# Performance work log

Measured on AMD Instinct MI355X. Metric: run time of the kernel, lower is better.

The kernel has to match this reference:

```python
import jax, jax.numpy as jnp
import numpy as np

B, T, K = 2048, 120, 128


def setup_inputs() -> dict:
    key = jax.random.key(0)
    k1, k2, k3 = jax.random.split(key, 3)
    emissions = jax.random.normal(k1, (B, T, K), dtype=jnp.float32)
    tag_ids = jax.random.randint(k2, (B, T), 0, K, dtype=jnp.int64)
    mask = jnp.ones((B, T), dtype=jnp.int32)  # full-length sequences
    # learned CRF transition weight (orthogonal-init stand-in: scaled normal)
    transitions = jax.random.normal(k3, (K, K), dtype=jnp.float32) * 0.1
    return {"emissions": emissions, "tag_ids": tag_ids, "mask": mask,
            "transitions": transitions}


def _crf_neg_log_likelihood(emissions, tag_ids, mask, transitions):
    maskf = mask.astype(emissions.dtype)  # [B,T]
    # ---- gold path score ----
    # unary: emission score of the gold tag at each valid position
    unary = jnp.take_along_axis(emissions, tag_ids[..., None], axis=2)[..., 0]  # [B,T]
    unary_score = jnp.sum(unary * maskf, axis=1)  # [B]
    # binary: transition score between consecutive gold tags (both positions valid)
    trans = transitions[tag_ids[:, :-1], tag_ids[:, 1:]]  # [B,T-1]
    pair_mask = maskf[:, :-1] * maskf[:, 1:]
    binary_score = jnp.sum(trans * pair_mask, axis=1)  # [B]
    score = unary_score + binary_score  # [B]

    # ---- log partition via forward algorithm (sequential scan over time) ----
    alpha0 = emissions[:, 0, :]  # [B,K]

    def step(alpha, xs):
        emis_t, mask_t = xs  # [B,K], [B]
        # alpha[b,i] + transitions[i,j] -> logsumexp over i, add emission at t
        new_alpha = jax.nn.logsumexp(alpha[:, :, None] + transitions[None, :, :],
                                     axis=1) + emis_t  # [B,K]
        alpha = jnp.where(mask_t[:, None] > 0, new_alpha, alpha)
        return alpha, None

    xs = (jnp.swapaxes(emissions[:, 1:, :], 0, 1),  # [T-1,B,K]
          jnp.swapaxes(mask[:, 1:], 0, 1))          # [T-1,B]
    alpha, _ = jax.lax.scan(step, alpha0, xs)
    log_norm = jax.nn.logsumexp(alpha, axis=1)  # [B]

    log_likelihood = score - log_norm  # [B]
    return -jnp.mean(log_likelihood)


def reference(emissions, tag_ids, mask, transitions):
    # CrfLossLayer.call computes the CRF NLL loss (added via add_loss);
    # the padded emissions/mask outputs are trivial zero-pads of the inputs.
    return _crf_neg_log_likelihood(emissions, tag_ids, mask, transitions)
```

## Files before the change

kernel.cpp:

```cpp
#include <hip/hip_runtime.h>
#include <cstddef>
#include <cstdint>

typedef __attribute__((ext_vector_type(8))) _Float16 half8;
typedef __attribute__((ext_vector_type(4))) float f32x4;

constexpr int Bsz = 2048, Tsz = 120, Ksz = 128;
constexpr float L2E = 1.44269504088896340736f;
constexpr float LN2 = 0.69314718055994530942f;

__device__ __forceinline__ int expbits(float x) {
  return (int)(__float_as_uint(x) >> 23) - 127;
}

#define BAR() do {                                        \
    asm volatile("s_waitcnt lgkmcnt(0)" ::: "memory");    \
    __builtin_amdgcn_s_barrier();                         \
    __builtin_amdgcn_sched_barrier(0);                    \
  } while (0)

__global__ __launch_bounds__(256) void crf_fwd(
    const float* __restrict__ emis,
    const int* __restrict__ tag,
    const int* __restrict__ maskg,
    const float* __restrict__ Tg,
    float* __restrict__ nll)
{
  __shared__ float Tst[Ksz * Ksz];
  __shared__ __align__(16) uint2 Pb[2][16 * 32];
  __shared__ __align__(16) float lamp[2][16][20];
  __shared__ int maskLds[Tsz * 16];

  const int tid = threadIdx.x;
  const int w = tid >> 6, lane = tid & 63;
  const int c = lane & 15, hi = lane >> 4;
  const int b0 = blockIdx.x * 16;
  const int sw2 = (c & 7) << 1;
  const int slot = 4 * w + hi;

  const int soff = 32 * w + 4 * hi;
  const float* ep = emis + (size_t)(b0 + c) * Tsz * Ksz + soff;

  f32x4 a0[2], emA[2], emB[2];
  a0[0] = *(const f32x4*)(ep);
  a0[1] = *(const f32x4*)(ep + 16);
  emA[0] = *(const f32x4*)(ep + Ksz);
  emA[1] = *(const f32x4*)(ep + Ksz + 16);
  emB[0] = *(const f32x4*)(ep + 2 * Ksz);
  emB[1] = *(const f32x4*)(ep + 2 * Ksz + 16);

  {
    const f32x4* src = (const f32x4*)Tg;
    f32x4* dst = (f32x4*)Tst;
    #pragma unroll
    for (int k = 0; k < (Ksz * Ksz / 4) / 256; ++k)
      dst[tid + k * 256] = src[tid + k * 256];
  }
  for (int i = tid; i < Tsz * 16; i += 256) {
    int cc = i & 15, tt = i >> 4;
    maskLds[i] = maskg[(size_t)(b0 + cc) * Tsz + tt];
  }
  __syncthreads();

  half8 Ef[2][4];
  #pragma unroll
  for (int rti = 0; rti < 2; ++rti)
    #pragma unroll
    for (int m = 0; m < 4; ++m) {
      half8 v;
      #pragma unroll
      for (int j = 0; j < 8; ++j)
        v[j] = (_Float16)__expf(Tst[(32 * m + 8 * hi + j) * Ksz + (32 * w + 16 * rti + c)]);
      Ef[rti][m] = v;
    }

  {
    float pm = fmaxf(fmaxf(fmaxf(a0[0][0], a0[0][1]), fmaxf(a0[0][2], a0[0][3])),
                     fmaxf(fmaxf(a0[1][0], a0[1][1]), fmaxf(a0[1][2], a0[1][3])));
    lamp[1][c][slot] = pm;
  }
  BAR();
  float nReg;
  f32x4 Pv[2];
  {
    const float* lr = &lamp[1][c][0];
    f32x4 l0 = *(const f32x4*)(lr), l1 = *(const f32x4*)(lr + 4);
    f32x4 l2 = *(const f32x4*)(lr + 8), l3 = *(const f32x4*)(lr + 12);
    f32x4 mm;
    #pragma unroll
    for (int r = 0; r < 4; ++r) mm[r] = fmaxf(fmaxf(l0[r], l1[r]), fmaxf(l2[r], l3[r]));
    float mx = fmaxf(fmaxf(mm[0], mm[1]), fmaxf(mm[2], mm[3]));
    nReg = mx * L2E;
    #pragma unroll
    for (int rti = 0; rti < 2; ++rti)
      #pragma unroll
      for (int r = 0; r < 4; ++r) Pv[rti][r] = __expf(a0[rti][r] - mx);
  }

  auto publish = [&](int wr) {
    float pl = 0.f;
    #pragma unroll
    for (int rti = 0; rti < 2; ++rti) {
      union { _Float16 h[4]; uint2 u; } pk;
      #pragma unroll
      for (int r = 0; r < 4; ++r) {
        pk.h[r] = (_Float16)Pv[rti][r];
        pl = fmaxf(pl, Pv[rti][r]);
      }
      Pb[wr][c * 32 + ((8 * w + 4 * rti + hi) ^ sw2)] = pk.u;
    }
    lamp[wr][c][slot] = pl;
  };

  publish(0);
  BAR();

  const f32x4 z = {0.f, 0.f, 0.f, 0.f};

  auto STEP = [&](int t, f32x4 (&em)[2]) {
    const int rd = (t - 1) & 1, wr = t & 1;
    const uint2* prowR = &Pb[rd][c * 32];
    half8 bf[4];
    #pragma unroll
    for (int m = 0; m < 4; ++m) {
      union { uint4 u4; half8 h; } rb;
      const int idx = (8 * m + 2 * hi) ^ sw2;
      rb.u4 = *(const uint4*)(&prowR[idx]);
      bf[m] = rb.h;
    }
    const float* lr = &lamp[rd][c][0];
    f32x4 l0 = *(const f32x4*)(lr), l1 = *(const f32x4*)(lr + 4);
    f32x4 l2 = *(const f32x4*)(lr + 8), l3 = *(const f32x4*)(lr + 12);
    f32x4 mm;
    #pragma unroll
    for (int r = 0; r < 4; ++r) mm[r] = fmaxf(fmaxf(l0[r], l1[r]), fmaxf(l2[r], l3[r]));
    const float lam = fmaxf(fmaxf(mm[0], mm[1]), fmaxf(mm[2], mm[3]));
    const int Dfi = expbits(lam) + 8;
    const float s2 = __uint_as_float((uint32_t)(127 - Dfi) << 23);
    const int mt = maskLds[t * 16 + c];

    f32x4 eem[2];
    #pragma unroll
    for (int rti = 0; rti < 2; ++rti)
      #pragma unroll
      for (int r = 0; r < 4; ++r) eem[rti][r] = __expf(em[rti][r]);

    f32x4 acc[2];
    #pragma unroll
    for (int rti = 0; rti < 2; ++rti) {
      f32x4 aA = __builtin_amdgcn_mfma_f32_16x16x32_f16(
          Ef[rti][1], bf[1],
          __builtin_amdgcn_mfma_f32_16x16x32_f16(Ef[rti][0], bf[0], z, 0, 0, 0),
          0, 0, 0);
      f32x4 aB = __builtin_amdgcn_mfma_f32_16x16x32_f16(
          Ef[rti][3], bf[3],
          __builtin_amdgcn_mfma_f32_16x16x32_f16(Ef[rti][2], bf[2], z, 0, 0, 0),
          0, 0, 0);
      #pragma unroll
      for (int r = 0; r < 4; ++r) acc[rti][r] = aA[r] + aB[r];
    }

    if (t + 2 < Tsz) {
      em[0] = *(const f32x4*)(ep + (size_t)(t + 2) * Ksz);
      em[1] = *(const f32x4*)(ep + (size_t)(t + 2) * Ksz + 16);
    }

    f32x4 c2[2];
    #pragma unroll
    for (int rti = 0; rti < 2; ++rti)
      #pragma unroll
      for (int r = 0; r < 4; ++r) c2[rti][r] = eem[rti][r] * s2;

    unsigned long long bal = __ballot(mt > 0);
    if (bal == ~0ull) {
      #pragma unroll
      for (int rti = 0; rti < 2; ++rti)
        #pragma unroll
        for (int r = 0; r < 4; ++r) Pv[rti][r] = acc[rti][r] * c2[rti][r];
    } else {
      #pragma unroll
      for (int rti = 0; rti < 2; ++rti)
        #pragma unroll
        for (int r = 0; r < 4; ++r) {
          float pn = acc[rti][r] * c2[rti][r];
          float po = Pv[rti][r] * s2;
          Pv[rti][r] = (mt > 0) ? pn : po;
        }
    }
    nReg += (float)Dfi;

    publish(wr);
    BAR();
  };

  #pragma unroll 1
  for (int t = 1; t <= Tsz - 3; t += 2) {
    STEP(t, emA);
    STEP(t + 1, emB);
  }
  STEP(Tsz - 1, emA);

  {
    float ss = ((Pv[0][0] + Pv[0][1]) + (Pv[0][2] + Pv[0][3]))
             + ((Pv[1][0] + Pv[1][1]) + (Pv[1][2] + Pv[1][3]));
    lamp[1][c][slot] = ss;
  }
  BAR();
  float lognorm;
  {
    const float* lr = &lamp[1][c][0];
    f32x4 l0 = *(const f32x4*)(lr), l1 = *(const f32x4*)(lr + 4);
    f32x4 l2 = *(const f32x4*)(lr + 8), l3 = *(const f32x4*)(lr + 12);
    float tot = (((l0[0] + l0[1]) + (l0[2] + l0[3]))
              + ((l1[0] + l1[1]) + (l1[2] + l1[3])))
              + (((l2[0] + l2[1]) + (l2[2] + l2[3]))
              + ((l3[0] + l3[1]) + (l3[2] + l3[3])));
    lognorm = nReg * LN2 + __logf(tot);
  }

  {
    const int* tb = tag + (size_t)(b0 + c) * Tsz;
    const float* eb2 = emis + (size_t)(b0 + c) * Tsz * Ksz;
    float sc = 0.f;
    const int t0 = 8 * slot;
    const int t1 = (t0 + 8 < Tsz) ? t0 + 8 : Tsz;
    #pragma unroll 1
    for (int t = t0; t < t1; ++t) {
      int tg0 = tb[t];
      float m0 = (float)maskLds[t * 16 + c];
      sc += eb2[(size_t)t * Ksz + tg0] * m0;
      if (t + 1 < Tsz) {
        int tg1 = tb[t + 1];
        sc += Tst[tg0 * Ksz + tg1] * m0 * (float)maskLds[(t + 1) * 16 + c];
      }
    }
    float* scb = (float*)&Pb[0][0];
    scb[c * 16 + slot] = sc;
    BAR();
    if (tid < 16) {
      const float* sr = &scb[c * 16];
      float s2r = 0.f;
      #pragma unroll
      for (int s = 0; s < 16; ++s) s2r += sr[s];
      nll[b0 + c] = lognorm - s2r;
    }
  }
}

__global__ __launch_bounds__(256) void crf_reduce(
    const float* __restrict__ nll, float* __restrict__ out) {
  __shared__ float buf[256];
  float s = 0.f;
  for (int i = threadIdx.x; i < Bsz; i += 256) s += nll[i];
  buf[threadIdx.x] = s;
  __syncthreads();
  #pragma unroll
  for (int off = 128; off > 0; off >>= 1) {
    if (threadIdx.x < off) buf[threadIdx.x] += buf[threadIdx.x + off];
    __syncthreads();
  }
  if (threadIdx.x == 0) out[0] = buf[0] / (float)Bsz;
}

extern "C" void kernel_launch(void* const* d_in, const int* in_sizes, int n_in,
                              void* d_out, int out_size, void* d_ws, size_t ws_size,
                              hipStream_t stream) {
  const float* emissions   = (const float*)d_in[0];
  const int*   tag_ids     = (const int*)d_in[1];
  const int*   mask        = (const int*)d_in[2];
  const float* transitions = (const float*)d_in[3];

  float* nll = (float*)d_ws;

  crf_fwd<<<Bsz / 16, 256, 0, stream>>>(emissions, tag_ids, mask, transitions, nll);
  crf_reduce<<<1, 256, 0, stream>>>(nll, (float*)d_out);
}
```

Before: 78.27 us.

## Halve block to two waves, each computing 64 tags per step

Each block now uses 128 threads (2 waves), and each wave covers 64 output tags with 4 MFMA column tiles instead of 2. This cuts the per-step barrier and LDS max-reduction cost, since 8 slots are reduced instead of 16. The transition matrix is no longer staged in LDS; the exp table and gold-path transition lookups read global memory directly. Emission loads are prefetched three steps ahead and their exp is computed before each step, which raises register pressure and halves the number of waves available per block.

```diff
diff --git a/kernel.cpp b/kernel.cpp
--- a/kernel.cpp
+++ b/kernel.cpp
@@ -16,19 +16,18 @@
 #define BAR() do {                                        \
     asm volatile("s_waitcnt lgkmcnt(0)" ::: "memory");    \
     __builtin_amdgcn_s_barrier();                         \
-    __builtin_amdgcn_sched_barrier(0);                    \
+    asm volatile("" ::: "memory");                        \
   } while (0)
 
-__global__ __launch_bounds__(256) void crf_fwd(
+__global__ __launch_bounds__(128, 1) void crf_fwd(
     const float* __restrict__ emis,
     const int* __restrict__ tag,
     const int* __restrict__ maskg,
     const float* __restrict__ Tg,
     float* __restrict__ nll)
 {
-  __shared__ float Tst[Ksz * Ksz];
   __shared__ __align__(16) uint2 Pb[2][16 * 32];
-  __shared__ __align__(16) float lamp[2][16][20];
+  __shared__ __align__(16) float lamp[2][16][10];
   __shared__ int maskLds[Tsz * 16];
 
   const int tid = threadIdx.x;
@@ -38,76 +37,76 @@
   const int sw2 = (c & 7) << 1;
   const int slot = 4 * w + hi;
 
-  const int soff = 32 * w + 4 * hi;
+  const int soff = 64 * w + 4 * hi;
   const float* ep = emis + (size_t)(b0 + c) * Tsz * Ksz + soff;
 
-  f32x4 a0[2], emA[2], emB[2];
-  a0[0] = *(const f32x4*)(ep);
-  a0[1] = *(const f32x4*)(ep + 16);
-  emA[0] = *(const f32x4*)(ep + Ksz);
-  emA[1] = *(const f32x4*)(ep + Ksz + 16);
-  emB[0] = *(const f32x4*)(ep + 2 * Ksz);
-  emB[1] = *(const f32x4*)(ep + 2 * Ksz + 16);
-
-  {
-    const f32x4* src = (const f32x4*)Tg;
-    f32x4* dst = (f32x4*)Tst;
-    #pragma unroll
-    for (int k = 0; k < (Ksz * Ksz / 4) / 256; ++k)
-      dst[tid + k * 256] = src[tid + k * 256];
-  }
-  for (int i = tid; i < Tsz * 16; i += 256) {
+  f32x4 a0[4], rT[4], rA[4], rB[4];
+  #pragma unroll
+  for (int qq = 0; qq < 4; ++qq) a0[qq] = *(const f32x4*)(ep + 16 * qq);
+  #pragma unroll
+  for (int qq = 0; qq < 4; ++qq) rT[qq] = *(const f32x4*)(ep + Ksz + 16 * qq);
+  #pragma unroll
+  for (int qq = 0; qq < 4; ++qq) rA[qq] = *(const f32x4*)(ep + 2 * Ksz + 16 * qq);
+  #pragma unroll
+  for (int qq = 0; qq < 4; ++qq) rB[qq] = *(const f32x4*)(ep + 3 * Ksz + 16 * qq);
+
+  for (int i = tid; i < Tsz * 16; i += 128) {
     int cc = i & 15, tt = i >> 4;
     maskLds[i] = maskg[(size_t)(b0 + cc) * Tsz + tt];
   }
-  __syncthreads();
-
-  half8 Ef[2][4];
-  #pragma unroll
-  for (int rti = 0; rti < 2; ++rti)
+
+  half8 Ef[4][4];
+  #pragma unroll
+  for (int qq = 0; qq < 4; ++qq)
     #pragma unroll
     for (int m = 0; m < 4; ++m) {
       half8 v;
       #pragma unroll
       for (int j = 0; j < 8; ++j)
-        v[j] = (_Float16)__expf(Tst[(32 * m + 8 * hi + j) * Ksz + (32 * w + 16 * rti + c)]);
-      Ef[rti][m] = v;
-    }
-
-  {
-    float pm = fmaxf(fmaxf(fmaxf(a0[0][0], a0[0][1]), fmaxf(a0[0][2], a0[0][3])),
-                     fmaxf(fmaxf(a0[1][0], a0[1][1]), fmaxf(a0[1][2], a0[1][3])));
+        v[j] = (_Float16)__expf(Tg[(size_t)(32 * m + 8 * hi + j) * Ksz + 64 * w + 16 * qq + c]);
+      Ef[qq][m] = v;
+    }
+
+  {
+    float pm = -3.0e38f;
+    #pragma unroll
+    for (int qq = 0; qq < 4; ++qq)
+      #pragma unroll
+      for (int r = 0; r < 4; ++r) pm = fmaxf(pm, a0[qq][r]);
     lamp[1][c][slot] = pm;
   }
   BAR();
   float nReg;
-  f32x4 Pv[2];
+  f32x4 Pv[4], eemA[4], eemB[4];
   {
     const float* lr = &lamp[1][c][0];
     f32x4 l0 = *(const f32x4*)(lr), l1 = *(const f32x4*)(lr + 4);
-    f32x4 l2 = *(const f32x4*)(lr + 8), l3 = *(const f32x4*)(lr + 12);
     f32x4 mm;
     #pragma unroll
-    for (int r = 0; r < 4; ++r) mm[r] = fmaxf(fmaxf(l0[r], l1[r]), fmaxf(l2[r], l3[r]));
+    for (int r = 0; r < 4; ++r) mm[r] = fmaxf(l0[r], l1[r]);
     float mx = fmaxf(fmaxf(mm[0], mm[1]), fmaxf(mm[2], mm[3]));
     nReg = mx * L2E;
     #pragma unroll
-    for (int rti = 0; rti < 2; ++rti)
-      #pragma unroll
-      for (int r = 0; r < 4; ++r) Pv[rti][r] = __expf(a0[rti][r] - mx);
+    for (int qq = 0; qq < 4; ++qq)
+      #pragma unroll
+      for (int r = 0; r < 4; ++r) Pv[qq][r] = __expf(a0[qq][r] - mx);
+    #pragma unroll
+    for (int qq = 0; qq < 4; ++qq)
+      #pragma unroll
+      for (int r = 0; r < 4; ++r) eemA[qq][r] = __expf(rT[qq][r]);
   }
 
   auto publish = [&](int wr) {
     float pl = 0.f;
     #pragma unroll
-    for (int rti = 0; rti < 2; ++rti) {
+    for (int qq = 0; qq < 4; ++qq) {
       union { _Float16 h[4]; uint2 u; } pk;
       #pragma unroll
       for (int r = 0; r < 4; ++r) {
-        pk.h[r] = (_Float16)Pv[rti][r];
-        pl = fmaxf(pl, Pv[rti][r]);
+        pk.h[r] = (_Float16)Pv[qq][r];
+        pl = fmaxf(pl, Pv[qq][r]);
       }
-      Pb[wr][c * 32 + ((8 * w + 4 * rti + hi) ^ sw2)] = pk.u;
+      Pb[wr][c * 32 + ((16 * w + 4 * qq + hi) ^ sw2)] = pk.u;
     }
     lamp[wr][c][slot] = pl;
   };
@@ -117,74 +116,61 @@
 
   const f32x4 z = {0.f, 0.f, 0.f, 0.f};
 
-  auto STEP = [&](int t, f32x4 (&em)[2]) {
+  auto STEP = [&](int t, f32x4 (&eemC)[4]) {
     const int rd = (t - 1) & 1, wr = t & 1;
     const uint2* prowR = &Pb[rd][c * 32];
     half8 bf[4];
     #pragma unroll
     for (int m = 0; m < 4; ++m) {
       union { uint4 u4; half8 h; } rb;
-      const int idx = (8 * m + 2 * hi) ^ sw2;
-      rb.u4 = *(const uint4*)(&prowR[idx]);
+      rb.u4 = *(const uint4*)(&prowR[(8 * m + 2 * hi) ^ sw2]);
       bf[m] = rb.h;
     }
     const float* lr = &lamp[rd][c][0];
     f32x4 l0 = *(const f32x4*)(lr), l1 = *(const f32x4*)(lr + 4);
-    f32x4 l2 = *(const f32x4*)(lr + 8), l3 = *(const f32x4*)(lr + 12);
     f32x4 mm;
     #pragma unroll
-    for (int r = 0; r < 4; ++r) mm[r] = fmaxf(fmaxf(l0[r], l1[r]), fmaxf(l2[r], l3[r]));
+    for (int r = 0; r < 4; ++r) mm[r] = fmaxf(l0[r], l1[r]);
     const float lam = fmaxf(fmaxf(mm[0], mm[1]), fmaxf(mm[2], mm[3]));
     const int Dfi = expbits(lam) + 8;
     const float s2 = __uint_as_float((uint32_t)(127 - Dfi) << 23);
     const int mt = maskLds[t * 16 + c];
 
-    f32x4 eem[2];
-    #pragma unroll
-    for (int rti = 0; rti < 2; ++rti)
-      #pragma unroll
-      for (int r = 0; r < 4; ++r) eem[rti][r] = __expf(em[rti][r]);
-
-    f32x4 acc[2];
-    #pragma unroll
-    for (int rti = 0; rti < 2; ++rti) {
+    f32x4 c2[4];
+    #pragma unroll
+    for (int qq = 0; qq < 4; ++qq)
+      #pragma unroll
+      for (int r = 0; r < 4; ++r) c2[qq][r] = eemC[qq][r] * s2;
+
+    f32x4 acc[4];
+    #pragma unroll
+    for (int qq = 0; qq < 4; ++qq) {
       f32x4 aA = __builtin_amdgcn_mfma_f32_16x16x32_f16(
-          Ef[rti][1], bf[1],
-          __builtin_amdgcn_mfma_f32_16x16x32_f16(Ef[rti][0], bf[0], z, 0, 0, 0),
+          Ef[qq][1], bf[1],
+          __builtin_amdgcn_mfma_f32_16x16x32_f16(Ef[qq][0], bf[0], z, 0, 0, 0),
           0, 0, 0);
       f32x4 aB = __builtin_amdgcn_mfma_f32_16x16x32_f16(
-          Ef[rti][3], bf[3],
-          __builtin_amdgcn_mfma_f32_16x16x32_f16(Ef[rti][2], bf[2], z, 0, 0, 0),
+          Ef[qq][3], bf[3],
+          __builtin_amdgcn_mfma_f32_16x16x32_f16(Ef[qq][2], bf[2], z, 0, 0, 0),
           0, 0, 0);
       #pragma unroll
-      for (int r = 0; r < 4; ++r) acc[rti][r] = aA[r] + aB[r];
-    }
-
-    if (t + 2 < Tsz) {
-      em[0] = *(const f32x4*)(ep + (size_t)(t + 2) * Ksz);
-      em[1] = *(const f32x4*)(ep + (size_t)(t + 2) * Ksz + 16);
-    }
-
-    f32x4 c2[2];
-    #pragma unroll
-    for (int rti = 0; rti < 2; ++rti)
-      #pragma unroll
-      for (int r = 0; r < 4; ++r) c2[rti][r] = eem[rti][r] * s2;
+      for (int r = 0; r < 4; ++r) acc[qq][r] = aA[r] + aB[r];
+    }
 
     unsigned long long bal = __ballot(mt > 0);
     if (bal == ~0ull) {
       #pragma unroll
-      for (int rti = 0; rti < 2; ++rti)
+      for (int qq = 0; qq < 4; ++qq)
         #pragma unroll
-        for (int r = 0; r < 4; ++r) Pv[rti][r] = acc[rti][r] * c2[rti][r];
+        for (int r = 0; r < 4; ++r) Pv[qq][r] = acc[qq][r] * c2[qq][r];
     } else {
       #pragma unroll
-      for (int rti = 0; rti < 2; ++rti)
+      for (int qq = 0; qq < 4; ++qq)
         #pragma unroll
         for (int r = 0; r < 4; ++r) {
-          float pn = acc[rti][r] * c2[rti][r];
-          float po = Pv[rti][r] * s2;
-          Pv[rti][r] = (mt > 0) ? pn : po;
+          float pn = acc[qq][r] * c2[qq][r];
+          float po = Pv[qq][r] * s2;
+          Pv[qq][r] = (mt > 0) ? pn : po;
         }
     }
     nReg += (float)Dfi;
@@ -195,26 +181,44 @@
 
   #pragma unroll 1
   for (int t = 1; t <= Tsz - 3; t += 2) {
-    STEP(t, emA);
-    STEP(t + 1, emB);
-  }
-  STEP(Tsz - 1, emA);
-
-  {
-    float ss = ((Pv[0][0] + Pv[0][1]) + (Pv[0][2] + Pv[0][3]))
-             + ((Pv[1][0] + Pv[1][1]) + (Pv[1][2] + Pv[1][3]));
-    lamp[1][c][slot] = ss;
+    #pragma unroll
+    for (int qq = 0; qq < 4; ++qq)
+      #pragma unroll
+      for (int r = 0; r < 4; ++r) eemB[qq][r] = __expf(rA[qq][r]);
+    STEP(t, eemA);
+    if (t + 3 < Tsz) {
+      #pragma unroll
+      for (int qq = 0; qq < 4; ++qq)
+        rA[qq] = *(const f32x4*)(ep + (size_t)(t + 3) * Ksz + 16 * qq);
+    }
+    #pragma unroll
+    for (int qq = 0; qq < 4; ++qq)
+      #pragma unroll
+      for (int r = 0; r < 4; ++r) eemA[qq][r] = __expf(rB[qq][r]);
+    STEP(t + 1, eemB);
+    if (t + 4 < Tsz) {
+      #pragma unroll
+      for (int qq = 0; qq < 4; ++qq)
+        rB[qq] = *(const f32x4*)(ep + (size_t)(t + 4) * Ksz + 16 * qq);
+    }
+  }
+  STEP(Tsz - 1, eemA);
+
+  {
+    float ss = 0.f;
+    #pragma unroll
+    for (int qq = 0; qq < 4; ++qq)
+      #pragma unroll
+      for (int r = 0; r < 4; ++r) ss += Pv[qq][r];
+    lamp[0][c][slot] = ss;
   }
   BAR();
   float lognorm;
   {
-    const float* lr = &lamp[1][c][0];
+    const float* lr = &lamp[0][c][0];
     f32x4 l0 = *(const f32x4*)(lr), l1 = *(const f32x4*)(lr + 4);
-    f32x4 l2 = *(const f32x4*)(lr + 8), l3 = *(const f32x4*)(lr + 12);
-    float tot = (((l0[0] + l0[1]) + (l0[2] + l0[3]))
-              + ((l1[0] + l1[1]) + (l1[2] + l1[3])))
-              + (((l2[0] + l2[1]) + (l2[2] + l2[3]))
-              + ((l3[0] + l3[1]) + (l3[2] + l3[3])));
+    float tot = ((l0[0] + l0[1]) + (l0[2] + l0[3]))
+              + ((l1[0] + l1[1]) + (l1[2] + l1[3]));
     lognorm = nReg * LN2 + __logf(tot);
   }
 
@@ -222,8 +226,7 @@
     const int* tb = tag + (size_t)(b0 + c) * Tsz;
     const float* eb2 = emis + (size_t)(b0 + c) * Tsz * Ksz;
     float sc = 0.f;
-    const int t0 = 8 * slot;
-    const int t1 = (t0 + 8 < Tsz) ? t0 + 8 : Tsz;
+    const int t0 = 15 * slot, t1 = t0 + 15;
     #pragma unroll 1
     for (int t = t0; t < t1; ++t) {
       int tg0 = tb[t];
@@ -231,17 +234,17 @@
       sc += eb2[(size_t)t * Ksz + tg0] * m0;
       if (t + 1 < Tsz) {
         int tg1 = tb[t + 1];
-        sc += Tst[tg0 * Ksz + tg1] * m0 * (float)maskLds[(t + 1) * 16 + c];
+        sc += Tg[(size_t)tg0 * Ksz + tg1] * m0 * (float)maskLds[(t + 1) * 16 + c];
       }
     }
     float* scb = (float*)&Pb[0][0];
-    scb[c * 16 + slot] = sc;
+    scb[c * 8 + slot] = sc;
     BAR();
     if (tid < 16) {
-      const float* sr = &scb[c * 16];
+      const float* sr = &scb[c * 8];
       float s2r = 0.f;
       #pragma unroll
-      for (int s = 0; s < 16; ++s) s2r += sr[s];
+      for (int s = 0; s < 8; ++s) s2r += sr[s];
       nll[b0 + c] = lognorm - s2r;
     }
   }
@@ -272,6 +275,6 @@
 
   float* nll = (float*)d_ws;
 
-  crf_fwd<<<Bsz / 16, 256, 0, stream>>>(emissions, tag_ids, mask, transitions, nll);
+  crf_fwd<<<Bsz / 16, 128, 0, stream>>>(emissions, tag_ids, mask, transitions, nll);
   crf_reduce<<<1, 256, 0, stream>>>(nll, (float*)d_out);
 }
```

Result: slower. 130.5 us (+66.8%).

## Shrink blocks to four sequences, use bf16 MFMA and precompute rescale one step ahead

Applied to the files above, without the earlier changes.

Each block now handles 4 batch rows instead of 16, giving four times as many blocks so more CUs are busy. The 16 MFMA columns are filled with 4 copies of each sequence. The per-step rescale factor and exp(emission) are now computed one step ahead from the previous step's max exponent, which takes the max-reduce-to-scale dependency off the serial chain. The kernel also switches from f16 to bf16 for the wider exponent range, and drops the LDS copy of the transition matrix in favour of direct global reads. The cost is redundant MFMA work on duplicated columns, and a lagged heuristic scale that may give weaker overflow control.

```diff
diff --git a/kernel.cpp b/kernel.cpp
--- a/kernel.cpp
+++ b/kernel.cpp
@@ -1,11 +1,13 @@
 #include <hip/hip_runtime.h>
+#include <hip/hip_bf16.h>
 #include <cstddef>
 #include <cstdint>
 
-typedef __attribute__((ext_vector_type(8))) _Float16 half8;
+typedef __attribute__((ext_vector_type(8))) short short8;
 typedef __attribute__((ext_vector_type(4))) float f32x4;
 
 constexpr int Bsz = 2048, Tsz = 120, Ksz = 128;
+constexpr int BPB = 4;
 constexpr float L2E = 1.44269504088896340736f;
 constexpr float LN2 = 0.69314718055994530942f;
 
@@ -16,7 +18,7 @@
 #define BAR() do {                                        \
     asm volatile("s_waitcnt lgkmcnt(0)" ::: "memory");    \
     __builtin_amdgcn_s_barrier();                         \
-    __builtin_amdgcn_sched_barrier(0);                    \
+    asm volatile("" ::: "memory");                        \
   } while (0)
 
 __global__ __launch_bounds__(256) void crf_fwd(
@@ -26,51 +28,45 @@
     const float* __restrict__ Tg,
     float* __restrict__ nll)
 {
-  __shared__ float Tst[Ksz * Ksz];
   __shared__ __align__(16) uint2 Pb[2][16 * 32];
   __shared__ __align__(16) float lamp[2][16][20];
-  __shared__ int maskLds[Tsz * 16];
+  __shared__ int maskLds[Tsz * BPB];
 
   const int tid = threadIdx.x;
   const int w = tid >> 6, lane = tid & 63;
   const int c = lane & 15, hi = lane >> 4;
-  const int b0 = blockIdx.x * 16;
+  const int bc = c & (BPB - 1);
+  const int b0 = blockIdx.x * BPB;
   const int sw2 = (c & 7) << 1;
   const int slot = 4 * w + hi;
 
   const int soff = 32 * w + 4 * hi;
-  const float* ep = emis + (size_t)(b0 + c) * Tsz * Ksz + soff;
-
-  f32x4 a0[2], emA[2], emB[2];
-  a0[0] = *(const f32x4*)(ep);
-  a0[1] = *(const f32x4*)(ep + 16);
-  emA[0] = *(const f32x4*)(ep + Ksz);
-  emA[1] = *(const f32x4*)(ep + Ksz + 16);
-  emB[0] = *(const f32x4*)(ep + 2 * Ksz);
-  emB[1] = *(const f32x4*)(ep + 2 * Ksz + 16);
-
-  {
-    const f32x4* src = (const f32x4*)Tg;
-    f32x4* dst = (f32x4*)Tst;
-    #pragma unroll
-    for (int k = 0; k < (Ksz * Ksz / 4) / 256; ++k)
-      dst[tid + k * 256] = src[tid + k * 256];
-  }
-  for (int i = tid; i < Tsz * 16; i += 256) {
-    int cc = i & 15, tt = i >> 4;
-    maskLds[i] = maskg[(size_t)(b0 + cc) * Tsz + tt];
-  }
-  __syncthreads();
-
-  half8 Ef[2][4];
+  const float* ep = emis + (size_t)(b0 + bc) * Tsz * Ksz + soff;
+
+  f32x4 a0[2], r1[2], rA[2], rB[2];
+  a0[0] = *(const f32x4*)(ep);           a0[1] = *(const f32x4*)(ep + 16);
+  r1[0] = *(const f32x4*)(ep + Ksz);     r1[1] = *(const f32x4*)(ep + Ksz + 16);
+  rA[0] = *(const f32x4*)(ep + 2 * Ksz); rA[1] = *(const f32x4*)(ep + 2 * Ksz + 16);
+  rB[0] = *(const f32x4*)(ep + 3 * Ksz); rB[1] = *(const f32x4*)(ep + 3 * Ksz + 16);
+
+  for (int i = tid; i < Tsz * BPB; i += 256) {
+    int bb = i & (BPB - 1), tt = i >> 2;
+    maskLds[i] = maskg[(size_t)(b0 + bb) * Tsz + tt];
+  }
+
+  short8 Ef[2][4];
   #pragma unroll
   for (int rti = 0; rti < 2; ++rti)
     #pragma unroll
     for (int m = 0; m < 4; ++m) {
-      half8 v;
-      #pragma unroll
-      for (int j = 0; j < 8; ++j)
-        v[j] = (_Float16)__expf(Tst[(32 * m + 8 * hi + j) * Ksz + (32 * w + 16 * rti + c)]);
+      short8 v;
+      #pragma unroll
+      for (int j = 0; j < 8; ++j) {
+        union { __hip_bfloat16 h; short s; } cv;
+        cv.h = __float2bfloat16(
+            __expf(Tg[(size_t)(32 * m + 8 * hi + j) * Ksz + 32 * w + 16 * rti + c]));
+        v[j] = cv.s;
+      }
       Ef[rti][m] = v;
     }
 
@@ -101,10 +97,10 @@
     float pl = 0.f;
     #pragma unroll
     for (int rti = 0; rti < 2; ++rti) {
-      union { _Float16 h[4]; uint2 u; } pk;
+      union { __hip_bfloat16 h[4]; uint2 u; } pk;
       #pragma unroll
       for (int r = 0; r < 4; ++r) {
-        pk.h[r] = (_Float16)Pv[rti][r];
+        pk.h[r] = __float2bfloat16(Pv[rti][r]);
         pl = fmaxf(pl, Pv[rti][r]);
       }
       Pb[wr][c * 32 + ((8 * w + 4 * rti + hi) ^ sw2)] = pk.u;
@@ -115,61 +111,42 @@
   publish(0);
   BAR();
 
-  const f32x4 z = {0.f, 0.f, 0.f, 0.f};
-
-  auto STEP = [&](int t, f32x4 (&em)[2]) {
+  const f32x4 z4 = {0.f, 0.f, 0.f, 0.f};
+
+  auto STEP = [&](int t, const f32x4 (&c2)[2], float s2, int Dfi, int& zOut) {
     const int rd = (t - 1) & 1, wr = t & 1;
     const uint2* prowR = &Pb[rd][c * 32];
-    half8 bf[4];
+    short8 bf[4];
     #pragma unroll
     for (int m = 0; m < 4; ++m) {
-      union { uint4 u4; half8 h; } rb;
-      const int idx = (8 * m + 2 * hi) ^ sw2;
-      rb.u4 = *(const uint4*)(&prowR[idx]);
+      union { uint4 u4; short8 h; } rb;
+      rb.u4 = *(const uint4*)(&prowR[(8 * m + 2 * hi) ^ sw2]);
       bf[m] = rb.h;
     }
     const float* lr = &lamp[rd][c][0];
     f32x4 l0 = *(const f32x4*)(lr), l1 = *(const f32x4*)(lr + 4);
     f32x4 l2 = *(const f32x4*)(lr + 8), l3 = *(const f32x4*)(lr + 12);
+    const int mt = maskLds[t * BPB + bc];
+
+    f32x4 acc[2];
+    #pragma unroll
+    for (int rti = 0; rti < 2; ++rti) {
+      f32x4 aA = __builtin_amdgcn_mfma_f32_16x16x32_bf16(
+          Ef[rti][1], bf[1],
+          __builtin_amdgcn_mfma_f32_16x16x32_bf16(Ef[rti][0], bf[0], z4, 0, 0, 0),
+          0, 0, 0);
+      f32x4 aB = __builtin_amdgcn_mfma_f32_16x16x32_bf16(
+          Ef[rti][3], bf[3],
+          __builtin_amdgcn_mfma_f32_16x16x32_bf16(Ef[rti][2], bf[2], z4, 0, 0, 0),
+          0, 0, 0);
+      #pragma unroll
+      for (int r = 0; r < 4; ++r) acc[rti][r] = aA[r] + aB[r];
+    }
+
     f32x4 mm;
     #pragma unroll
     for (int r = 0; r < 4; ++r) mm[r] = fmaxf(fmaxf(l0[r], l1[r]), fmaxf(l2[r], l3[r]));
-    const float lam = fmaxf(fmaxf(mm[0], mm[1]), fmaxf(mm[2], mm[3]));
-    const int Dfi = expbits(lam) + 8;
-    const float s2 = __uint_as_float((uint32_t)(127 - Dfi) << 23);
-    const int mt = maskLds[t * 16 + c];
-
-    f32x4 eem[2];
-    #pragma unroll
-    for (int rti = 0; rti < 2; ++rti)
-      #pragma unroll
-      for (int r = 0; r < 4; ++r) eem[rti][r] = __expf(em[rti][r]);
-
-    f32x4 acc[2];
-    #pragma unroll
-    for (int rti = 0; rti < 2; ++rti) {
-      f32x4 aA = __builtin_amdgcn_mfma_f32_16x16x32_f16(
-          Ef[rti][1], bf[1],
-          __builtin_amdgcn_mfma_f32_16x16x32_f16(Ef[rti][0], bf[0], z, 0, 0, 0),
-          0, 0, 0);
-      f32x4 aB = __builtin_amdgcn_mfma_f32_16x16x32_f16(
-          Ef[rti][3], bf[3],
-          __builtin_amdgcn_mfma_f32_16x16x32_f16(Ef[rti][2], bf[2], z, 0, 0, 0),
-          0, 0, 0);
-      #pragma unroll
-      for (int r = 0; r < 4; ++r) acc[rti][r] = aA[r] + aB[r];
-    }
-
-    if (t + 2 < Tsz) {
-      em[0] = *(const f32x4*)(ep + (size_t)(t + 2) * Ksz);
-      em[1] = *(const f32x4*)(ep + (size_t)(t + 2) * Ksz + 16);
-    }
-
-    f32x4 c2[2];
-    #pragma unroll
-    for (int rti = 0; rti < 2; ++rti)
-      #pragma unroll
-      for (int r = 0; r < 4; ++r) c2[rti][r] = eem[rti][r] * s2;
+    zOut = expbits(fmaxf(fmaxf(mm[0], mm[1]), fmaxf(mm[2], mm[3])));
 
     unsigned long long bal = __ballot(mt > 0);
     if (bal == ~0ull) {
@@ -193,22 +170,64 @@
     BAR();
   };
 
+  int DfA = 7;
+  float s2A = __uint_as_float((uint32_t)(127 - 7) << 23);
+  f32x4 c2A[2], c2B[2];
+  #pragma unroll
+  for (int rti = 0; rti < 2; ++rti)
+    #pragma unroll
+    for (int r = 0; r < 4; ++r) c2A[rti][r] = __expf(r1[rti][r]) * s2A;
+
+  int zCur;
   #pragma unroll 1
   for (int t = 1; t <= Tsz - 3; t += 2) {
-    STEP(t, emA);
-    STEP(t + 1, emB);
-  }
-  STEP(Tsz - 1, emA);
+    f32x4 eB[2];
+    #pragma unroll
+    for (int rti = 0; rti < 2; ++rti)
+      #pragma unroll
+      for (int r = 0; r < 4; ++r) eB[rti][r] = __expf(rA[rti][r]);
+    STEP(t, c2A, s2A, DfA, zCur);
+    int DfB = 7 + (zCur >> 2);
+    DfB = DfB < -90 ? -90 : (DfB > 110 ? 110 : DfB);
+    float s2B = __uint_as_float((uint32_t)(127 - DfB) << 23);
+    #pragma unroll
+    for (int rti = 0; rti < 2; ++rti)
+      #pragma unroll
+      for (int r = 0; r < 4; ++r) c2B[rti][r] = eB[rti][r] * s2B;
+    if (t + 3 < Tsz) {
+      rA[0] = *(const f32x4*)(ep + (size_t)(t + 3) * Ksz);
+      rA[1] = *(const f32x4*)(ep + (size_t)(t + 3) * Ksz + 16);
+    }
+
+    f32x4 eA[2];
+    #pragma unroll
+    for (int rti = 0; rti < 2; ++rti)
+      #pragma unroll
+      for (int r = 0; r < 4; ++r) eA[rti][r] = __expf(rB[rti][r]);
+    STEP(t + 1, c2B, s2B, DfB, zCur);
+    DfA = 7 + (zCur >> 2);
+    DfA = DfA < -90 ? -90 : (DfA > 110 ? 110 : DfA);
+    s2A = __uint_as_float((uint32_t)(127 - DfA) << 23);
+    #pragma unroll
+    for (int rti = 0; rti < 2; ++rti)
+      #pragma unroll
+      for (int r = 0; r < 4; ++r) c2A[rti][r] = eA[rti][r] * s2A;
+    if (t + 4 < Tsz) {
+      rB[0] = *(const f32x4*)(ep + (size_t)(t + 4) * Ksz);
+      rB[1] = *(const f32x4*)(ep + (size_t)(t + 4) * Ksz + 16);
+    }
+  }
+  STEP(Tsz - 1, c2A, s2A, DfA, zCur);
 
   {
     float ss = ((Pv[0][0] + Pv[0][1]) + (Pv[0][2] + Pv[0][3]))
              + ((Pv[1][0] + Pv[1][1]) + (Pv[1][2] + Pv[1][3]));
-    lamp[1][c][slot] = ss;
+    lamp[0][c][slot] = ss;
   }
   BAR();
   float lognorm;
   {
-    const float* lr = &lamp[1][c][0];
+    const float* lr = &lamp[0][c][0];
     f32x4 l0 = *(const f32x4*)(lr), l1 = *(const f32x4*)(lr + 4);
     f32x4 l2 = *(const f32x4*)(lr + 8), l3 = *(const f32x4*)(lr + 12);
     float tot = (((l0[0] + l0[1]) + (l0[2] + l0[3]))
@@ -219,30 +238,30 @@
   }
 
   {
-    const int* tb = tag + (size_t)(b0 + c) * Tsz;
-    const float* eb2 = emis + (size_t)(b0 + c) * Tsz * Ksz;
+    const int* tb = tag + (size_t)(b0 + bc) * Tsz;
+    const float* eb2 = emis + (size_t)(b0 + bc) * Tsz * Ksz;
     float sc = 0.f;
     const int t0 = 8 * slot;
     const int t1 = (t0 + 8 < Tsz) ? t0 + 8 : Tsz;
     #pragma unroll 1
     for (int t = t0; t < t1; ++t) {
       int tg0 = tb[t];
-      float m0 = (float)maskLds[t * 16 + c];
+      float m0 = (float)maskLds[t * BPB + bc];
       sc += eb2[(size_t)t * Ksz + tg0] * m0;
       if (t + 1 < Tsz) {
         int tg1 = tb[t + 1];
-        sc += Tst[tg0 * Ksz + tg1] * m0 * (float)maskLds[(t + 1) * 16 + c];
+        sc += Tg[(size_t)tg0 * Ksz + tg1] * m0 * (float)maskLds[(t + 1) * BPB + bc];
       }
     }
     float* scb = (float*)&Pb[0][0];
-    scb[c * 16 + slot] = sc;
+    scb[bc * 16 + slot] = sc;
     BAR();
-    if (tid < 16) {
-      const float* sr = &scb[c * 16];
+    if (tid < BPB) {
+      const float* sr = &scb[tid * 16];
       float s2r = 0.f;
       #pragma unroll
       for (int s = 0; s < 16; ++s) s2r += sr[s];
-      nll[b0 + c] = lognorm - s2r;
+      nll[b0 + tid] = lognorm - s2r;
     }
   }
 }
@@ -272,6 +291,6 @@
 
   float* nll = (float*)d_ws;
 
-  crf_fwd<<<Bsz / 16, 256, 0, stream>>>(emissions, tag_ids, mask, transitions, nll);
+  crf_fwd<<<Bsz / BPB, 256, 0, stream>>>(emissions, tag_ids, mask, transitions, nll);
   crf_reduce<<<1, 256, 0, stream>>>(nll, (float*)d_out);
 }
```

New measurement: 110.9 us. +41.7%, slower.
